# Kernel optimization log

Hardware: AMD Instinct MI355X
Metric: run time of the kernel (lower is better)

Reference implementation:

```python
import jax, jax.numpy as jnp
import numpy as np

VOCAB, D, H = 100000, 128, 256
B, T = 64, 512


def setup_inputs() -> dict:
    key = jax.random.key(0)
    ks = jax.random.split(key, 7)
    path = jax.random.randint(ks[0], (B, T), 0, VOCAB, dtype=jnp.int32)
    valid_len = jax.random.randint(ks[1], (B,), 1, T + 1, dtype=jnp.int32)
    embedding = jax.random.normal(ks[2], (VOCAB, D), dtype=jnp.float32)
    s_ih = 1.0 / np.sqrt(H)
    W_ih = jax.random.uniform(ks[3], (4 * H, D), jnp.float32, -s_ih, s_ih)
    W_hh = jax.random.uniform(ks[4], (4 * H, H), jnp.float32, -s_ih, s_ih)
    b_ih = jax.random.uniform(ks[5], (4 * H,), jnp.float32, -s_ih, s_ih)
    b_hh = jax.random.uniform(ks[6], (4 * H,), jnp.float32, -s_ih, s_ih)
    return {"path": path, "valid_len": valid_len, "embedding": embedding,
            "W_ih": W_ih, "W_hh": W_hh, "b_ih": b_ih, "b_hh": b_hh}


def _lstm_last(x, valid_len, W_ih, W_hh, b_ih, b_hh):
    # x: [B, T, D] -> last-valid hidden state [B, H]
    Bx, Tx, _ = x.shape
    Hd = W_hh.shape[1]
    # precompute input projections for all steps: [T, B, 4H]
    xp = jnp.einsum('btd,gd->tbg', x, W_ih) + b_ih + b_hh

    def step(carry, xg):
        h, c = carry
        gates = xg + h @ W_hh.T  # [B, 4H]
        i, f, g, o = jnp.split(gates, 4, axis=-1)  # pytorch gate order i,f,g,o
        c = jax.nn.sigmoid(f) * c + jax.nn.sigmoid(i) * jnp.tanh(g)
        h = jax.nn.sigmoid(o) * jnp.tanh(c)
        return (h, c), h

    h0 = jnp.zeros((Bx, Hd), x.dtype)
    c0 = jnp.zeros((Bx, Hd), x.dtype)
    _, hs = jax.lax.scan(step, (h0, c0), xp)  # hs: [T, B, H]
    # gather output at t = valid_len - 1 (packed LSTM never advances past valid_len)
    return hs[valid_len - 1, jnp.arange(Bx)]


def reference(path, valid_len, embedding, W_ih, W_hh, b_ih, b_hh):
    x = embedding[path]  # [B, T, D] irregular gather
    return _lstm_last(x, valid_len, W_ih, W_hh, b_ih, b_hh)
```

## Files before the change

kernel.cpp:

```cpp
#include <hip/hip_runtime.h>
#include <stdint.h>


#define BB 64
#define TT 512
#define DD 128
#define HH 256

typedef __fp16 half2v __attribute__((ext_vector_type(2)));

__device__ __forceinline__ uint32_t pk_f16(float lo, float hi) {
    half2v h = __builtin_amdgcn_cvt_pkrtz(lo, hi);
    return __builtin_bit_cast(uint32_t, h);
}

__device__ __forceinline__ float dot2(uint32_t a, uint32_t b, float acc) {
#if __has_builtin(__builtin_amdgcn_fdot2)
    return __builtin_amdgcn_fdot2(__builtin_bit_cast(half2v, a),
                                  __builtin_bit_cast(half2v, b), acc, false);
#else
    half2v av = __builtin_bit_cast(half2v, a);
    half2v bv = __builtin_bit_cast(half2v, b);
    acc += (float)av[0] * (float)bv[0];
    acc += (float)av[1] * (float)bv[1];
    return acc;
#endif
}

__device__ __forceinline__ float fsig(float x)  { return 1.f / (1.f + __expf(-x)); }
__device__ __forceinline__ float ftanh(float x) { return 1.f - 2.f / (__expf(2.f * x) + 1.f); }

__global__ __launch_bounds__(1024, 4)
void lstm_cluster_kernel(const int* __restrict__ path, const int* __restrict__ vlen,
                         const float* __restrict__ emb, const float* __restrict__ Wih,
                         const float* __restrict__ Whh, const float* __restrict__ bih,
                         const float* __restrict__ bhh, float* __restrict__ out,
                         uint32_t* hx ) {
    const int b   = blockIdx.x & (BB - 1);
    const int k   = blockIdx.x >> 6;
    const int tid = threadIdx.x;
    const int r   = tid >> 2;
    const int q   = tid & 3;
    const int g   = r >> 6;
    const int u   = r & 63;
    const int grow = (g << 8) + (k << 6) + u;

    __shared__ uint32_t h_pk[4][40];
    __shared__ uint32_t x_pk[2][4][24];
    __shared__ float    G[256];
    __shared__ int      path_l[TT];

    uint32_t whh[32];
    {
        const float* wr = Whh + grow * HH + (q << 6);
#pragma unroll
        for (int c = 0; c < 32; ++c) whh[c] = pk_f16(wr[2 * c], wr[2 * c + 1]);
    }
    uint32_t wih[16];
    {
        const float* wr = Wih + grow * DD + (q << 5);
#pragma unroll
        for (int c = 0; c < 16; ++c) wih[c] = pk_f16(wr[2 * c], wr[2 * c + 1]);
    }
    const float bias = bih[grow] + bhh[grow];
    const int   L    = vlen[b];

    if (tid < TT)  path_l[tid] = path[b * TT + tid];
    if (tid < 160) ((uint32_t*)h_pk)[tid] = 0u;
    __syncthreads();

    float xr_next = 0.f;
    if (tid >= 128 && tid < 256) {
        int e = tid - 128;
        float x0 = emb[(size_t)path_l[0] * DD + e];
        float hi = __shfl_xor(x0, 1);
        if (!(e & 1)) x_pk[0][e >> 5][(e & 31) >> 1] = pk_f16(x0, hi);
        xr_next = emb[(size_t)path_l[L > 1 ? 1 : 0] * DD + e];
    }
    float c_state = 0.f;
    __syncthreads();

    for (int t = 0; t < L; ++t) {
        const int slot  = t & 1;
        const int phase = (t >> 1) & 1;
        const uint32_t want = phase ? 0x40004000u : 0u;

        float acc = 0.f;
#pragma unroll
        for (int c = 0; c < 8; ++c) {
            uint4 hv = *(const uint4*)&h_pk[q][c << 2];
            acc = dot2(whh[(c << 2) + 0], hv.x, acc);
            acc = dot2(whh[(c << 2) + 1], hv.y, acc);
            acc = dot2(whh[(c << 2) + 2], hv.z, acc);
            acc = dot2(whh[(c << 2) + 3], hv.w, acc);
        }
#pragma unroll
        for (int c = 0; c < 4; ++c) {
            uint4 xv = *(const uint4*)&x_pk[slot][q][c << 2];
            acc = dot2(wih[(c << 2) + 0], xv.x, acc);
            acc = dot2(wih[(c << 2) + 1], xv.y, acc);
            acc = dot2(wih[(c << 2) + 2], xv.z, acc);
            acc = dot2(wih[(c << 2) + 3], xv.w, acc);
        }
        acc += __shfl_xor(acc, 1);
        acc += __shfl_xor(acc, 2);
        if (q == 0) G[r] = acc + bias;
        __syncthreads();

        if (tid < 64) {
            float gi = fsig(G[tid]);
            float gf = fsig(G[64 + tid]);
            float gg = ftanh(G[128 + tid]);
            float go = fsig(G[192 + tid]);
            c_state  = gf * c_state + gi * gg;
            float h  = go * ftanh(c_state);
            if (t == L - 1) out[b * HH + (k << 6) + tid] = h;
            float h1 = __shfl_xor(h, 1);
            if (!(tid & 1)) {
                uint32_t pk = pk_f16(h, h1);
                h_pk[k][tid >> 1] = pk;
                __hip_atomic_store(&hx[(slot * BB + b) * 128 + (k << 5) + (tid >> 1)],
                                   phase ? ~pk : pk,
                                   __ATOMIC_RELAXED, __HIP_MEMORY_SCOPE_AGENT);
            }
        } else if (tid >= 128 && tid < 256) {
            int e = tid - 128;
            float hi = __shfl_xor(xr_next, 1);
            if (!(e & 1)) x_pk[slot ^ 1][e >> 5][(e & 31) >> 1] = pk_f16(xr_next, hi);
            int tpf = (t + 2 < TT) ? t + 2 : TT - 1;
            xr_next = emb[(size_t)path_l[tpf] * DD + e];
        } else if (tid >= 896 && tid < 992 && t < L - 1) {
            int j  = tid - 896;
            int qq = j >> 5; if (qq >= k) ++qq;
            int c  = j & 31;
            uint32_t* addr = &hx[(slot * BB + b) * 128 + (qq << 5) + c];
            uint32_t v; int spins = 0;
            do {
                v = __hip_atomic_load(addr, __ATOMIC_RELAXED, __HIP_MEMORY_SCOPE_AGENT);
            } while ((v & 0x40004000u) != want && ++spins < (1 << 20));
            h_pk[qq][c] = phase ? ~v : v;
        }
        __syncthreads();
    }
}

extern "C" void kernel_launch(void* const* d_in, const int* in_sizes, int n_in,
                              void* d_out, int out_size, void* d_ws, size_t ws_size,
                              hipStream_t stream) {
    const int*   path = (const int*)d_in[0];
    const int*   vlen = (const int*)d_in[1];
    const float* emb  = (const float*)d_in[2];
    const float* Wih  = (const float*)d_in[3];
    const float* Whh  = (const float*)d_in[4];
    const float* bih  = (const float*)d_in[5];
    const float* bhh  = (const float*)d_in[6];

    (void)hipMemsetAsync(d_ws, 0xFF, (size_t)2 * BB * 128 * sizeof(uint32_t), stream);
    lstm_cluster_kernel<<<256, 1024, 0, stream>>>(path, vlen, emb, Wih, Whh, bih, bhh,
                                                  (float*)d_out, (uint32_t*)d_ws);
}
```

Baseline: 679.5 us.

## Remap matvec to 4 rows per thread with DPP reductions and sc0 fast exchange

Each thread now computes four gate rows over a 16-column slice, reusing the h and x vectors loaded from LDS across rows, and reduces across 16 lanes with DPP adds instead of two shuffles. The cross-block hidden-state exchange gains a second buffer that is written and polled with sc0 global loads and stores in inline asm. This is meant as a lower-latency path than agent-scope atomics. A bounded spin falls back to the atomic buffer if the fast path stalls. The aim is to cut per-step latency in the serial recurrence, at the cost of relying on the sc0 cache-coherence behaviour and doubling the store traffic.

```diff
diff --git a/kernel.cpp b/kernel.cpp
--- a/kernel.cpp
+++ b/kernel.cpp
@@ -27,6 +27,22 @@
 #endif
 }
 
+template<int CTRL>
+__device__ __forceinline__ float dpp_add(float a) {
+    int m = __builtin_amdgcn_update_dpp(0, __builtin_bit_cast(int, a), CTRL, 0xF, 0xF, false);
+    return a + __builtin_bit_cast(float, m);
+}
+
+__device__ __forceinline__ uint32_t load_sc0(const uint32_t* p) {
+    uint32_t v;
+    asm volatile("global_load_dword %0, %1, off sc0\n\ts_waitcnt vmcnt(0)"
+                 : "=v"(v) : "v"(p) : "memory");
+    return v;
+}
+__device__ __forceinline__ void store_sc0(uint32_t* p, uint32_t v) {
+    asm volatile("global_store_dword %0, %1, off sc0" :: "v"(p), "v"(v) : "memory");
+}
+
 __device__ __forceinline__ float fsig(float x)  { return 1.f / (1.f + __expf(-x)); }
 __device__ __forceinline__ float ftanh(float x) { return 1.f - 2.f / (__expf(2.f * x) + 1.f); }
 
@@ -35,38 +51,37 @@
                          const float* __restrict__ emb, const float* __restrict__ Wih,
                          const float* __restrict__ Whh, const float* __restrict__ bih,
                          const float* __restrict__ bhh, float* __restrict__ out,
-                         uint32_t* hx ) {
+                         uint32_t* hxF ,
+                         uint32_t* hxA ) {
     const int b   = blockIdx.x & (BB - 1);
     const int k   = blockIdx.x >> 6;
     const int tid = threadIdx.x;
-    const int r   = tid >> 2;
-    const int q   = tid & 3;
-    const int g   = r >> 6;
-    const int u   = r & 63;
-    const int grow = (g << 8) + (k << 6) + u;
-
-    __shared__ uint32_t h_pk[4][40];
-    __shared__ uint32_t x_pk[2][4][24];
+    const int rg  = tid >> 4;
+    const int cg  = tid & 15;
+
+    __shared__ uint32_t h_pk[16][12];
+    __shared__ uint32_t x_pk[2][16][12];
     __shared__ float    G[256];
     __shared__ int      path_l[TT];
 
-    uint32_t whh[32];
-    {
-        const float* wr = Whh + grow * HH + (q << 6);
-#pragma unroll
-        for (int c = 0; c < 32; ++c) whh[c] = pk_f16(wr[2 * c], wr[2 * c + 1]);
+    uint32_t whh[32], wih[16];
+    float    bias[4];
+#pragma unroll
+    for (int rr = 0; rr < 4; ++rr) {
+        const int row  = (rg << 2) + rr;
+        const int grow = ((row >> 6) << 8) + (k << 6) + (row & 63);
+        const float* wr = Whh + grow * HH + (cg << 4);
+#pragma unroll
+        for (int c = 0; c < 8; ++c) whh[rr * 8 + c] = pk_f16(wr[2 * c], wr[2 * c + 1]);
+        const float* wr2 = Wih + grow * DD + (cg << 3);
+#pragma unroll
+        for (int c = 0; c < 4; ++c) wih[rr * 4 + c] = pk_f16(wr2[2 * c], wr2[2 * c + 1]);
+        bias[rr] = bih[grow] + bhh[grow];
     }
-    uint32_t wih[16];
-    {
-        const float* wr = Wih + grow * DD + (q << 5);
-#pragma unroll
-        for (int c = 0; c < 16; ++c) wih[c] = pk_f16(wr[2 * c], wr[2 * c + 1]);
-    }
-    const float bias = bih[grow] + bhh[grow];
-    const int   L    = vlen[b];
+    const int L = vlen[b];
 
     if (tid < TT)  path_l[tid] = path[b * TT + tid];
-    if (tid < 160) ((uint32_t*)h_pk)[tid] = 0u;
+    if (tid < 192) ((uint32_t*)h_pk)[tid] = 0u;
     __syncthreads();
 
     float xr_next = 0.f;
@@ -74,10 +89,11 @@
         int e = tid - 128;
         float x0 = emb[(size_t)path_l[0] * DD + e];
         float hi = __shfl_xor(x0, 1);
-        if (!(e & 1)) x_pk[0][e >> 5][(e & 31) >> 1] = pk_f16(x0, hi);
+        if (!(e & 1)) { int j = e >> 1; x_pk[0][j >> 2][j & 3] = pk_f16(x0, hi); }
         xr_next = emb[(size_t)path_l[L > 1 ? 1 : 0] * DD + e];
     }
     float c_state = 0.f;
+    bool  fast_ok = true;
     __syncthreads();
 
     for (int t = 0; t < L; ++t) {
@@ -85,26 +101,32 @@
         const int phase = (t >> 1) & 1;
         const uint32_t want = phase ? 0x40004000u : 0u;
 
-        float acc = 0.f;
-#pragma unroll
-        for (int c = 0; c < 8; ++c) {
-            uint4 hv = *(const uint4*)&h_pk[q][c << 2];
-            acc = dot2(whh[(c << 2) + 0], hv.x, acc);
-            acc = dot2(whh[(c << 2) + 1], hv.y, acc);
-            acc = dot2(whh[(c << 2) + 2], hv.z, acc);
-            acc = dot2(whh[(c << 2) + 3], hv.w, acc);
+        const uint4 hv0 = *(const uint4*)&h_pk[cg][0];
+        const uint4 hv1 = *(const uint4*)&h_pk[cg][4];
+        const uint4 xv  = *(const uint4*)&x_pk[slot][cg][0];
+        float acc[4];
+#pragma unroll
+        for (int rr = 0; rr < 4; ++rr) {
+            float a = 0.f;
+            a = dot2(whh[rr * 8 + 0], hv0.x, a);
+            a = dot2(whh[rr * 8 + 1], hv0.y, a);
+            a = dot2(whh[rr * 8 + 2], hv0.z, a);
+            a = dot2(whh[rr * 8 + 3], hv0.w, a);
+            a = dot2(whh[rr * 8 + 4], hv1.x, a);
+            a = dot2(whh[rr * 8 + 5], hv1.y, a);
+            a = dot2(whh[rr * 8 + 6], hv1.z, a);
+            a = dot2(whh[rr * 8 + 7], hv1.w, a);
+            a = dot2(wih[rr * 4 + 0], xv.x, a);
+            a = dot2(wih[rr * 4 + 1], xv.y, a);
+            a = dot2(wih[rr * 4 + 2], xv.z, a);
+            a = dot2(wih[rr * 4 + 3], xv.w, a);
+            a = dpp_add<0xB1>(a);
+            a = dpp_add<0x4E>(a);
+            a = dpp_add<0x124>(a);
+            a = dpp_add<0x128>(a);
+            acc[rr] = a + bias[rr];
         }
-#pragma unroll
-        for (int c = 0; c < 4; ++c) {
-            uint4 xv = *(const uint4*)&x_pk[slot][q][c << 2];
-            acc = dot2(wih[(c << 2) + 0], xv.x, acc);
-            acc = dot2(wih[(c << 2) + 1], xv.y, acc);
-            acc = dot2(wih[(c << 2) + 2], xv.z, acc);
-            acc = dot2(wih[(c << 2) + 3], xv.w, acc);
-        }
-        acc += __shfl_xor(acc, 1);
-        acc += __shfl_xor(acc, 2);
-        if (q == 0) G[r] = acc + bias;
+        if (cg == 0) *(float4*)&G[rg << 2] = make_float4(acc[0], acc[1], acc[2], acc[3]);
         __syncthreads();
 
         if (tid < 64) {
@@ -118,27 +140,44 @@
             float h1 = __shfl_xor(h, 1);
             if (!(tid & 1)) {
                 uint32_t pk = pk_f16(h, h1);
-                h_pk[k][tid >> 1] = pk;
-                __hip_atomic_store(&hx[(slot * BB + b) * 128 + (k << 5) + (tid >> 1)],
-                                   phase ? ~pk : pk,
+                int jj = (k << 5) + (tid >> 1);
+                h_pk[jj >> 3][jj & 7] = pk;
+                uint32_t enc = phase ? ~pk : pk;
+                int idx = (slot * BB + b) * 128 + jj;
+                store_sc0(hxF + idx, enc);
+                __hip_atomic_store(hxA + idx, enc,
                                    __ATOMIC_RELAXED, __HIP_MEMORY_SCOPE_AGENT);
             }
         } else if (tid >= 128 && tid < 256) {
             int e = tid - 128;
             float hi = __shfl_xor(xr_next, 1);
-            if (!(e & 1)) x_pk[slot ^ 1][e >> 5][(e & 31) >> 1] = pk_f16(xr_next, hi);
+            if (!(e & 1)) { int j = e >> 1; x_pk[slot ^ 1][j >> 2][j & 3] = pk_f16(xr_next, hi); }
             int tpf = (t + 2 < TT) ? t + 2 : TT - 1;
             xr_next = emb[(size_t)path_l[tpf] * DD + e];
         } else if (tid >= 896 && tid < 992 && t < L - 1) {
             int j  = tid - 896;
             int qq = j >> 5; if (qq >= k) ++qq;
             int c  = j & 31;
-            uint32_t* addr = &hx[(slot * BB + b) * 128 + (qq << 5) + c];
-            uint32_t v; int spins = 0;
-            do {
-                v = __hip_atomic_load(addr, __ATOMIC_RELAXED, __HIP_MEMORY_SCOPE_AGENT);
-            } while ((v & 0x40004000u) != want && ++spins < (1 << 20));
-            h_pk[qq][c] = phase ? ~v : v;
+            const int idx = (slot * BB + b) * 128 + (qq << 5) + c;
+            uint32_t v; bool got = false;
+            if (fast_ok) {
+                int bound = (t == 0) ? 5000 : 1000;
+                do {
+                    v = load_sc0(hxF + idx);
+                    got = ((v & 0x40004000u) == want);
+                } while (!got && --bound);
+                if (!got) fast_ok = false;
+            }
+            if (!got) {
+                int spins = 0;
+                do {
+                    v = __hip_atomic_load(hxA + idx, __ATOMIC_RELAXED,
+                                          __HIP_MEMORY_SCOPE_AGENT);
+                } while ((v & 0x40004000u) != want && ++spins < (1 << 20));
+            }
+            uint32_t d = phase ? ~v : v;
+            int jj = (qq << 5) + c;
+            h_pk[jj >> 3][jj & 7] = d;
         }
         __syncthreads();
     }
@@ -155,7 +194,9 @@
     const float* bih  = (const float*)d_in[5];
     const float* bhh  = (const float*)d_in[6];
 
-    (void)hipMemsetAsync(d_ws, 0xFF, (size_t)2 * BB * 128 * sizeof(uint32_t), stream);
+    uint32_t* hxA = (uint32_t*)d_ws;
+    uint32_t* hxF = hxA + 2 * BB * 128;
+    (void)hipMemsetAsync(d_ws, 0xFF, (size_t)4 * BB * 128 * sizeof(uint32_t), stream);
     lstm_cluster_kernel<<<256, 1024, 0, stream>>>(path, vlen, emb, Wih, Whh, bih, bhh,
-                                                  (float*)d_out, (uint32_t*)d_ws);
-}
+                                                  (float*)d_out, hxF, hxA);
+}
```

Measured after the change: 1.237 ms. +82.0%, slower.

## Split each sequence's LSTM across eight blocks of 512 threads instead of four

Applied to the files above, without the earlier changes.

Each batch row's recurrence is now spread over 8 cooperating workgroups (32 hidden units each) instead of 4 (64 units each). Each thread computes two gate rows over a 32-wide slice with 8-lane reductions done through DPP adds instead of shuffles. The bias is folded into the activation step, and the spin-wait exchange of h through global memory now covers 7 peers. The goal is a shorter per-step critical path (fewer dot products per thread, smaller blocks). The cost is more cross-block synchronisation traffic and a dependence on all 512 blocks being co-resident for the spin-waits.

```diff
diff --git a/kernel.cpp b/kernel.cpp
--- a/kernel.cpp
+++ b/kernel.cpp
@@ -9,72 +9,83 @@
 
 typedef __fp16 half2v __attribute__((ext_vector_type(2)));
 
-__device__ __forceinline__ uint32_t pk_f16(float lo, float hi) {
+static __device__ __forceinline__ uint32_t pk_f16(float lo, float hi) {
     half2v h = __builtin_amdgcn_cvt_pkrtz(lo, hi);
     return __builtin_bit_cast(uint32_t, h);
 }
-
-__device__ __forceinline__ float dot2(uint32_t a, uint32_t b, float acc) {
-#if __has_builtin(__builtin_amdgcn_fdot2)
+static __device__ __forceinline__ uint4 pk4(const float* p) {
+    return make_uint4(pk_f16(p[0], p[1]), pk_f16(p[2], p[3]),
+                      pk_f16(p[4], p[5]), pk_f16(p[6], p[7]));
+}
+static __device__ __forceinline__ float dot2(uint32_t a, uint32_t b, float acc) {
     return __builtin_amdgcn_fdot2(__builtin_bit_cast(half2v, a),
                                   __builtin_bit_cast(half2v, b), acc, false);
-#else
-    half2v av = __builtin_bit_cast(half2v, a);
-    half2v bv = __builtin_bit_cast(half2v, b);
-    acc += (float)av[0] * (float)bv[0];
-    acc += (float)av[1] * (float)bv[1];
-    return acc;
-#endif
+}
+static __device__ __forceinline__ float dot8(uint4 w, uint4 v, float a) {
+    a = dot2(w.x, v.x, a); a = dot2(w.y, v.y, a);
+    a = dot2(w.z, v.z, a); a = dot2(w.w, v.w, a);
+    return a;
 }
 
-__device__ __forceinline__ float fsig(float x)  { return 1.f / (1.f + __expf(-x)); }
-__device__ __forceinline__ float ftanh(float x) { return 1.f - 2.f / (__expf(2.f * x) + 1.f); }
+template<int CTRL>
+static __device__ __forceinline__ float dpp_add(float a) {
+    int m = __builtin_amdgcn_update_dpp(0, __builtin_bit_cast(int, a), CTRL, 0xF, 0xF, false);
+    return a + __builtin_bit_cast(float, m);
+}
 
-__global__ __launch_bounds__(1024, 4)
-void lstm_cluster_kernel(const int* __restrict__ path, const int* __restrict__ vlen,
-                         const float* __restrict__ emb, const float* __restrict__ Wih,
-                         const float* __restrict__ Whh, const float* __restrict__ bih,
-                         const float* __restrict__ bhh, float* __restrict__ out,
-                         uint32_t* hx ) {
-    const int b   = blockIdx.x & (BB - 1);
-    const int k   = blockIdx.x >> 6;
+static __device__ __forceinline__ float fsig(float x)  { return 1.f / (1.f + __expf(-x)); }
+static __device__ __forceinline__ float ftanh(float x) { return 1.f - 2.f / (__expf(2.f * x) + 1.f); }
+
+__global__ __launch_bounds__(512)
+void lstm_oct_kernel(const int* __restrict__ path, const int* __restrict__ vlen,
+                     const float* __restrict__ emb, const float* __restrict__ Wih,
+                     const float* __restrict__ Whh, const float* __restrict__ bih,
+                     const float* __restrict__ bhh, float* __restrict__ out,
+                     uint32_t* hx ) {
+    const int b   = blockIdx.x >> 3;
+    const int k   = blockIdx.x & 7;
     const int tid = threadIdx.x;
-    const int r   = tid >> 2;
-    const int q   = tid & 3;
-    const int g   = r >> 6;
-    const int u   = r & 63;
-    const int grow = (g << 8) + (k << 6) + u;
+    const int cg  = tid & 7;
+    const int rb  = tid >> 3;
 
-    __shared__ uint32_t h_pk[4][40];
-    __shared__ uint32_t x_pk[2][4][24];
-    __shared__ float    G[256];
+    __shared__ uint32_t h_pk[8][20];
+    __shared__ uint32_t x_pk[2][8][12];
+    __shared__ float    G[128];
     __shared__ int      path_l[TT];
 
-    uint32_t whh[32];
-    {
-        const float* wr = Whh + grow * HH + (q << 6);
-#pragma unroll
-        for (int c = 0; c < 32; ++c) whh[c] = pk_f16(wr[2 * c], wr[2 * c + 1]);
+    const int r0 = rb << 1, r1 = r0 | 1;
+    const int grow0 = ((r0 >> 5) << 8) + (k << 5) + (r0 & 31);
+    const int grow1 = ((r1 >> 5) << 8) + (k << 5) + (r1 & 31);
+    const float* wp0 = Whh + grow0 * HH + (cg << 5);
+    const float* wp1 = Whh + grow1 * HH + (cg << 5);
+    const uint4 wh0a = pk4(wp0),      wh0b = pk4(wp0 + 8),
+                wh0c = pk4(wp0 + 16), wh0d = pk4(wp0 + 24);
+    const uint4 wh1a = pk4(wp1),      wh1b = pk4(wp1 + 8),
+                wh1c = pk4(wp1 + 16), wh1d = pk4(wp1 + 24);
+    const float* xp0 = Wih + grow0 * DD + (cg << 4);
+    const float* xp1 = Wih + grow1 * DD + (cg << 4);
+    const uint4 wx0a = pk4(xp0), wx0b = pk4(xp0 + 8);
+    const uint4 wx1a = pk4(xp1), wx1b = pk4(xp1 + 8);
+    const int L = vlen[b];
+
+    float bi = 0.f, bf = 0.f, bg = 0.f, bo = 0.f;
+    if (tid < 32) {
+        const int u = (k << 5) + tid;
+        bi = bih[u]       + bhh[u];
+        bf = bih[256 + u] + bhh[256 + u];
+        bg = bih[512 + u] + bhh[512 + u];
+        bo = bih[768 + u] + bhh[768 + u];
     }
-    uint32_t wih[16];
-    {
-        const float* wr = Wih + grow * DD + (q << 5);
-#pragma unroll
-        for (int c = 0; c < 16; ++c) wih[c] = pk_f16(wr[2 * c], wr[2 * c + 1]);
-    }
-    const float bias = bih[grow] + bhh[grow];
-    const int   L    = vlen[b];
-
-    if (tid < TT)  path_l[tid] = path[b * TT + tid];
+    path_l[tid] = path[b * TT + tid];
     if (tid < 160) ((uint32_t*)h_pk)[tid] = 0u;
     __syncthreads();
 
     float xr_next = 0.f;
-    if (tid >= 128 && tid < 256) {
-        int e = tid - 128;
-        float x0 = emb[(size_t)path_l[0] * DD + e];
-        float hi = __shfl_xor(x0, 1);
-        if (!(e & 1)) x_pk[0][e >> 5][(e & 31) >> 1] = pk_f16(x0, hi);
+    if (tid >= 384) {
+        int e = tid - 384;
+        float x0  = emb[(size_t)path_l[0] * DD + e];
+        float x0h = __shfl_xor(x0, 1);
+        if (!(e & 1)) x_pk[0][e >> 4][(e >> 1) & 7] = pk_f16(x0, x0h);
         xr_next = emb[(size_t)path_l[L > 1 ? 1 : 0] * DD + e];
     }
     float c_state = 0.f;
@@ -85,60 +96,58 @@
         const int phase = (t >> 1) & 1;
         const uint32_t want = phase ? 0x40004000u : 0u;
 
-        float acc = 0.f;
-#pragma unroll
-        for (int c = 0; c < 8; ++c) {
-            uint4 hv = *(const uint4*)&h_pk[q][c << 2];
-            acc = dot2(whh[(c << 2) + 0], hv.x, acc);
-            acc = dot2(whh[(c << 2) + 1], hv.y, acc);
-            acc = dot2(whh[(c << 2) + 2], hv.z, acc);
-            acc = dot2(whh[(c << 2) + 3], hv.w, acc);
-        }
-#pragma unroll
-        for (int c = 0; c < 4; ++c) {
-            uint4 xv = *(const uint4*)&x_pk[slot][q][c << 2];
-            acc = dot2(wih[(c << 2) + 0], xv.x, acc);
-            acc = dot2(wih[(c << 2) + 1], xv.y, acc);
-            acc = dot2(wih[(c << 2) + 2], xv.z, acc);
-            acc = dot2(wih[(c << 2) + 3], xv.w, acc);
-        }
-        acc += __shfl_xor(acc, 1);
-        acc += __shfl_xor(acc, 2);
-        if (q == 0) G[r] = acc + bias;
+        const uint4 hv0 = *(const uint4*)&h_pk[cg][0];
+        const uint4 hv1 = *(const uint4*)&h_pk[cg][4];
+        const uint4 hv2 = *(const uint4*)&h_pk[cg][8];
+        const uint4 hv3 = *(const uint4*)&h_pk[cg][12];
+        const uint4 xv0 = *(const uint4*)&x_pk[slot][cg][0];
+        const uint4 xv1 = *(const uint4*)&x_pk[slot][cg][4];
+        float a0 = 0.f, a1 = 0.f;
+        a0 = dot8(wh0a, hv0, a0); a0 = dot8(wh0b, hv1, a0);
+        a0 = dot8(wh0c, hv2, a0); a0 = dot8(wh0d, hv3, a0);
+        a0 = dot8(wx0a, xv0, a0); a0 = dot8(wx0b, xv1, a0);
+        a1 = dot8(wh1a, hv0, a1); a1 = dot8(wh1b, hv1, a1);
+        a1 = dot8(wh1c, hv2, a1); a1 = dot8(wh1d, hv3, a1);
+        a1 = dot8(wx1a, xv0, a1); a1 = dot8(wx1b, xv1, a1);
+        a0 = dpp_add<0xB1>(a0); a0 = dpp_add<0x4E>(a0); a0 = dpp_add<0x141>(a0);
+        a1 = dpp_add<0xB1>(a1); a1 = dpp_add<0x4E>(a1); a1 = dpp_add<0x141>(a1);
+        if (cg == 0) *(float2*)&G[r0] = make_float2(a0, a1);
         __syncthreads();
 
-        if (tid < 64) {
-            float gi = fsig(G[tid]);
-            float gf = fsig(G[64 + tid]);
-            float gg = ftanh(G[128 + tid]);
-            float go = fsig(G[192 + tid]);
+        if (tid < 32) {
+            float gi = fsig(G[tid] + bi);
+            float gf = fsig(G[32 + tid] + bf);
+            float gg = ftanh(G[64 + tid] + bg);
+            float go = fsig(G[96 + tid] + bo);
             c_state  = gf * c_state + gi * gg;
             float h  = go * ftanh(c_state);
-            if (t == L - 1) out[b * HH + (k << 6) + tid] = h;
+            if (t == L - 1) out[b * HH + (k << 5) + tid] = h;
             float h1 = __shfl_xor(h, 1);
             if (!(tid & 1)) {
                 uint32_t pk = pk_f16(h, h1);
-                h_pk[k][tid >> 1] = pk;
-                __hip_atomic_store(&hx[(slot * BB + b) * 128 + (k << 5) + (tid >> 1)],
+                int j = (k << 4) + (tid >> 1);
+                h_pk[j >> 4][j & 15] = pk;
+                __hip_atomic_store(&hx[(slot * BB + b) * 128 + j],
                                    phase ? ~pk : pk,
                                    __ATOMIC_RELAXED, __HIP_MEMORY_SCOPE_AGENT);
             }
-        } else if (tid >= 128 && tid < 256) {
-            int e = tid - 128;
-            float hi = __shfl_xor(xr_next, 1);
-            if (!(e & 1)) x_pk[slot ^ 1][e >> 5][(e & 31) >> 1] = pk_f16(xr_next, hi);
+        } else if (tid >= 64 && tid < 176) {
+            if (t < L - 1) {
+                int jj = tid - 64;
+                int j  = jj + (jj >= (k << 4) ? 16 : 0);
+                uint32_t* addr = &hx[(slot * BB + b) * 128 + j];
+                uint32_t v; int spins = 0;
+                do {
+                    v = __hip_atomic_load(addr, __ATOMIC_RELAXED, __HIP_MEMORY_SCOPE_AGENT);
+                } while ((v & 0x40004000u) != want && ++spins < (1 << 20));
+                h_pk[j >> 4][j & 15] = phase ? ~v : v;
+            }
+        } else if (tid >= 384) {
+            int e = tid - 384;
+            float xh = __shfl_xor(xr_next, 1);
+            if (!(e & 1)) x_pk[slot ^ 1][e >> 4][(e >> 1) & 7] = pk_f16(xr_next, xh);
             int tpf = (t + 2 < TT) ? t + 2 : TT - 1;
             xr_next = emb[(size_t)path_l[tpf] * DD + e];
-        } else if (tid >= 896 && tid < 992 && t < L - 1) {
-            int j  = tid - 896;
-            int qq = j >> 5; if (qq >= k) ++qq;
-            int c  = j & 31;
-            uint32_t* addr = &hx[(slot * BB + b) * 128 + (qq << 5) + c];
-            uint32_t v; int spins = 0;
-            do {
-                v = __hip_atomic_load(addr, __ATOMIC_RELAXED, __HIP_MEMORY_SCOPE_AGENT);
-            } while ((v & 0x40004000u) != want && ++spins < (1 << 20));
-            h_pk[qq][c] = phase ? ~v : v;
         }
         __syncthreads();
     }
@@ -156,6 +165,6 @@
     const float* bhh  = (const float*)d_in[6];
 
     (void)hipMemsetAsync(d_ws, 0xFF, (size_t)2 * BB * 128 * sizeof(uint32_t), stream);
-    lstm_cluster_kernel<<<256, 1024, 0, stream>>>(path, vlen, emb, Wih, Whh, bih, bhh,
-                                                  (float*)d_out, (uint32_t*)d_ws);
+    lstm_oct_kernel<<<512, 512, 0, stream>>>(path, vlen, emb, Wih, Whh, bih, bhh,
+                                             (float*)d_out, (uint32_t*)d_ws);
 }
```

After: 890.4 us. 1.31x slower.
